# Kernel optimization log

Measured on AMD Instinct MI355X. Metric: run time of the kernel, lower is better.

Reference implementation:

```python
import math
import jax, jax.numpy as jnp
import numpy as np

B, C, H, W = 8, 512, 32, 32
NUM_HEADS = 8
HEAD_DIM = C // NUM_HEADS


def setup_inputs() -> dict:
    key = jax.random.key(0)
    ks = jax.random.split(key, 5)
    scale = 1.0 / math.sqrt(C)
    return {
        "x": jax.random.normal(ks[0], (B, C, H, W), dtype=jnp.float32),
        "Wq": jax.random.normal(ks[1], (C, C), dtype=jnp.float32) * scale,
        "bq": jnp.zeros((C,), dtype=jnp.float32),
        "Wk": jax.random.normal(ks[2], (C, C), dtype=jnp.float32) * scale,
        "bk": jnp.zeros((C,), dtype=jnp.float32),
        "Wv": jax.random.normal(ks[3], (C, C), dtype=jnp.float32) * scale,
        "bv": jnp.zeros((C,), dtype=jnp.float32),
        "Wo": jax.random.normal(ks[4], (C, C), dtype=jnp.float32) * scale,
        "bo": jnp.zeros((C,), dtype=jnp.float32),
    }


def reference(x, Wq, bq, Wk, bk, Wv, bv, Wo, bo):
    b, c, h, w = x.shape
    t = h * w
    # (B,C,H,W) -> (B,T,C) token sequence
    xt = x.reshape(b, c, t).transpose(0, 2, 1)
    Q = xt @ Wq + bq
    K = xt @ Wk + bk
    V = xt @ Wv + bv
    # (B,T,C) -> (B,nh,T,hd)
    def split_heads(z):
        return z.reshape(b, t, NUM_HEADS, HEAD_DIM).transpose(0, 2, 1, 3)
    Qh, Kh, Vh = split_heads(Q), split_heads(K), split_heads(V)
    S = jnp.einsum("bhqd,bhkd->bhqk", Qh, Kh) / math.sqrt(HEAD_DIM)
    A = jax.nn.softmax(S, axis=-1)  # dropout p=0.0 -> identity
    Y = jnp.einsum("bhqk,bhkd->bhqd", A, Vh)
    Y = Y.transpose(0, 2, 1, 3).reshape(b, t, c)
    O = Y @ Wo + bo
    out = xt + O
    return out.transpose(0, 2, 1).reshape(b, c, h, w)
```

## Files before the change

### kernel.cpp

```cpp
#include <hip/hip_runtime.h>
#include <hip/hip_bf16.h>

#define B_  8
#define C_  512
#define T_  1024
#define NH_ 8
#define HD_ 64

#define QSCALE 0.1803368801111243f

using short8 = __attribute__((ext_vector_type(8))) short;
using f32x4  = __attribute__((ext_vector_type(4))) float;
using f32x16 = __attribute__((ext_vector_type(16))) float;
using us4    = __attribute__((ext_vector_type(4))) unsigned short;

__device__ __forceinline__ unsigned short f2bf(float f) {
    unsigned u = __builtin_bit_cast(unsigned, f);
    u += 0x7fff + ((u >> 16) & 1);
    return (unsigned short)(u >> 16);
}
__device__ __forceinline__ unsigned pack2bf(float lo, float hi) {
    __hip_bfloat162 h = __float22bfloat162_rn(float2{lo, hi});
    unsigned u;
    __builtin_memcpy(&u, &h, 4);
    return u;
}

__device__ __forceinline__ void gload_lds16(const ushort* g, ushort* l) {
    __builtin_amdgcn_global_load_lds(
        (const __attribute__((address_space(1))) void*)g,
        (__attribute__((address_space(3))) void*)l, 16, 0, 0);
}

template <int N>
__device__ __forceinline__ void wait_vmcnt() {
    asm volatile("s_waitcnt vmcnt(%0)" ::"n"(N) : "memory");
    __builtin_amdgcn_sched_barrier(0);
}
__device__ __forceinline__ void barrier_raw() {
    __builtin_amdgcn_sched_barrier(0);
    __builtin_amdgcn_s_barrier();
}

__global__ __launch_bounds__(256) void k_prep(const float* __restrict__ x,
                                              const float* __restrict__ Wq,
                                              const float* __restrict__ Wk,
                                              const float* __restrict__ Wv,
                                              const float* __restrict__ Wo,
                                              ushort* __restrict__ xt,
                                              ushort* __restrict__ Wqkvt,
                                              ushort* __restrict__ Wot) {
    __shared__ float tile[32][33];
    int L = blockIdx.x;
    int tx = threadIdx.x & 31, ty = threadIdx.x >> 5;
    if (L < 4096) {
        int b = L >> 9, rem = L & 511;
        int t0 = (rem & 31) * 32, c0 = (rem >> 5) * 32;
#pragma unroll
        for (int i = 0; i < 4; i++)
            tile[ty + i * 8][tx] = x[((size_t)b * C_ + c0 + ty + i * 8) * T_ + t0 + tx];
        __syncthreads();
#pragma unroll
        for (int i = 0; i < 4; i++)
            xt[((size_t)b * T_ + t0 + ty + i * 8) * C_ + c0 + tx] = f2bf(tile[tx][ty + i * 8]);
    } else {
        int LL = L - 4096;
        int m = LL >> 8, rem = LL & 255;
        int k0 = (rem & 15) * 32, n0 = (rem >> 4) * 32;
        const float* W = (m == 0) ? Wq : (m == 1) ? Wk : (m == 2) ? Wv : Wo;
        ushort* dst = (m < 3) ? (Wqkvt + (size_t)m * C_ * C_) : Wot;
        float scale = (m == 0) ? QSCALE : 1.0f;
#pragma unroll
        for (int i = 0; i < 4; i++)
            tile[ty + i * 8][tx] = W[(size_t)(k0 + ty + i * 8) * C_ + n0 + tx];
        __syncthreads();
#pragma unroll
        for (int i = 0; i < 4; i++)
            dst[(size_t)(n0 + ty + i * 8) * C_ + k0 + tx] = f2bf(tile[tx][ty + i * 8] * scale);
    }
}

__device__ __forceinline__ void gemm_core(const ushort* __restrict__ A,
                                          const ushort* __restrict__ Bt,
                                          int row0, int col0, int tid,
                                          ushort (*As)[8192], ushort (*Bs)[8192],
                                          f32x4 acc[4][4]) {
    f32x4 zero = {0.f, 0.f, 0.f, 0.f};
#pragma unroll
    for (int i = 0; i < 4; i++)
#pragma unroll
        for (int j = 0; j < 4; j++) acc[i][j] = zero;
    int lane = tid & 63, w = tid >> 6;
    int ql = lane & 15, g = lane >> 4;
    int wm = (w >> 1) * 64, wn = (w & 1) * 64;
    int srow = lane >> 3;
    int scol8 = (lane & 7) ^ (srow & 7);

#pragma unroll
    for (int i = 0; i < 4; i++) {
        int c = w * 4 + i;
        int r = c * 8 + srow;
        gload_lds16(A + (size_t)(row0 + r) * C_ + scol8 * 8, As[0] + c * 512);
        gload_lds16(Bt + (size_t)(col0 + r) * C_ + scol8 * 8, Bs[0] + c * 512);
    }

#pragma unroll
    for (int kt = 0; kt < 8; kt++) {
        int cur = kt & 1;
        if (kt < 7) {
            int k0 = (kt + 1) * 64;
#pragma unroll
            for (int i = 0; i < 4; i++) {
                int c = w * 4 + i;
                int r = c * 8 + srow;
                gload_lds16(A + (size_t)(row0 + r) * C_ + k0 + scol8 * 8, As[cur ^ 1] + c * 512);
                gload_lds16(Bt + (size_t)(col0 + r) * C_ + k0 + scol8 * 8, Bs[cur ^ 1] + c * 512);
            }
            wait_vmcnt<8>();
        } else {
            wait_vmcnt<0>();
        }
        barrier_raw();
        const ushort* Ac = As[cur];
        const ushort* Bc = Bs[cur];
        __builtin_amdgcn_s_setprio(1);
#pragma unroll
        for (int s = 0; s < 2; s++) {
            short8 a[4], b[4];
            int cs = ((4 * s + g) ^ (ql & 7)) * 8;
#pragma unroll
            for (int mt = 0; mt < 4; mt++)
                a[mt] = *(const short8*)(Ac + (wm + mt * 16 + ql) * 64 + cs);
#pragma unroll
            for (int nt = 0; nt < 4; nt++)
                b[nt] = *(const short8*)(Bc + (wn + nt * 16 + ql) * 64 + cs);
#pragma unroll
            for (int mt = 0; mt < 4; mt++)
#pragma unroll
                for (int nt = 0; nt < 4; nt++)
                    acc[mt][nt] = __builtin_amdgcn_mfma_f32_16x16x32_bf16(
                        a[mt], b[nt], acc[mt][nt], 0, 0, 0);
        }
        __builtin_amdgcn_s_setprio(0);
        barrier_raw();
    }
}

__global__ __launch_bounds__(256) void k_qkv(const ushort* __restrict__ xt,
                                             const ushort* __restrict__ Wqkvt,
                                             const float* __restrict__ bq,
                                             const float* __restrict__ bk,
                                             const float* __restrict__ bv,
                                             ushort* __restrict__ Qh,
                                             ushort* __restrict__ Kh,
                                             ushort* __restrict__ Vt) {
    __shared__ __align__(16) ushort As[2][8192];
    __shared__ __align__(16) ushort Bs[2][8192];
    f32x4 acc[4][4];
    int tid = threadIdx.x;
    int L = blockIdx.x;
    int n = L >> 3, xcd = L & 7;
    int row0 = (xcd * 8 + (n & 7)) * 128;
    int col0 = (n >> 3) * 128;
    gemm_core(xt, Wqkvt, row0, col0, tid, As, Bs, acc);
    int lane = tid & 63, w = tid >> 6;
    int ql = lane & 15, g = lane >> 4;
    int wm = (w >> 1) * 64, wn = (w & 1) * 64;
    int which = col0 >> 9;
    const float* bias = (which == 0) ? bq : (which == 1) ? bk : bv;
    float bscale = (which == 0) ? QSCALE : 1.0f;
    ushort* Lt = &As[0][0];

    if (which < 3 && which != 2) {
        ushort* dst = (which == 0) ? Qh : Kh;
#pragma unroll
        for (int mt = 0; mt < 4; mt++)
#pragma unroll
            for (int nt = 0; nt < 4; nt++) {
                int col = wn + nt * 16 + ql;
                float bsv = bias[(col0 + col) & 511] * bscale;
#pragma unroll
                for (int r = 0; r < 4; r++) {
                    int row = wm + mt * 16 + 4 * g + r;
                    int sw = col ^ ((row & 7) << 3);
                    Lt[row * 128 + sw] = f2bf(acc[mt][nt][r] + bsv);
                }
            }
        __syncthreads();
#pragma unroll
        for (int i = 0; i < 8; i++) {
            int task = w * 512 + i * 64 + lane;
            int row = task >> 4, gran = task & 15;
            int sg = gran ^ (row & 7);
            short8 vle = *(const short8*)(Lt + row * 128 + sg * 8);
            int gcol = col0 + gran * 8;
            int hc = gcol & 511, h = hc >> 6, d = hc & 63;
            int grow = row0 + row, b = grow >> 10, t = grow & 1023;
            *(short8*)(dst + ((size_t)(b * NH_ + h) * T_ + t) * HD_ + d) = vle;
        }
    } else {
#pragma unroll
        for (int mt = 0; mt < 4; mt++)
#pragma unroll
            for (int nt = 0; nt < 4; nt++) {
                int col = wn + nt * 16 + ql;
                float bsv = bias[(col0 + col) & 511] * bscale;
                int rowb = wm + mt * 16 + 4 * g;
                int swz = (rowb >> 2) ^ (col & 31);
                us4 pk;
#pragma unroll
                for (int r = 0; r < 4; r++) pk[r] = f2bf(acc[mt][nt][r] + bsv);
                *(us4*)(Lt + col * 128 + swz * 4) = pk;
            }
        __syncthreads();
#pragma unroll
        for (int i = 0; i < 8; i++) {
            int task = w * 512 + i * 64 + lane;
            int colr = task >> 4, gran = task & 15;
            int g4a = (2 * gran) ^ (colr & 31);
            int g4b = (2 * gran + 1) ^ (colr & 31);
            us4 lo = *(const us4*)(Lt + colr * 128 + g4a * 4);
            us4 hi4 = *(const us4*)(Lt + colr * 128 + g4b * 4);
            us4 arr[2] = {lo, hi4};
            short8 vle;
            __builtin_memcpy(&vle, arr, 16);
            int gcol = col0 + colr;
            int hc = gcol & 511, h = hc >> 6, d = hc & 63;
            int grow = row0 + gran * 8, b = grow >> 10, t = grow & 1023;
            *(short8*)(Vt + ((size_t)(b * NH_ + h) * HD_ + d) * T_ + t) = vle;
        }
    }
}

__global__ __launch_bounds__(256) void k_attn(const ushort* __restrict__ Qh,
                                              const ushort* __restrict__ Kh,
                                              const ushort* __restrict__ Vt,
                                              ushort* __restrict__ Y) {
    __shared__ __align__(16) ushort KV[4][4096];
    int tid = threadIdx.x, lane = tid & 63, w = tid >> 6;
    int hi = lane >> 5, l31 = lane & 31, l7 = lane & 7;
    int bh = blockIdx.x & 63, q0 = (blockIdx.x >> 6) * 128;
    int b = bh >> 3, h = bh & 7;
    int srow = lane >> 3;
    int scol8 = l7 ^ (srow & 7);
    const ushort* Kbase = Kh + (size_t)bh * T_ * HD_;
    const ushort* Vbase = Vt + (size_t)bh * HD_ * T_;
    const ushort* kv = &KV[0][0];

    short8 qa[4];
#pragma unroll
    for (int s = 0; s < 4; s++)
        qa[s] = *(const short8*)(Qh + ((size_t)bh * T_ + q0 + w * 32 + l31) * HD_ +
                                 s * 16 + hi * 8);

    int fofs[4];
#pragma unroll
    for (int s = 0; s < 4; s++) fofs[s] = ((2 * s + hi) ^ l7) * 8;
    int rowlo = l31 * 64;

    short8 ones;
    {
        short ov = (l31 == 0) ? (short)0x3F80 : (short)0;
#pragma unroll
        for (int j = 0; j < 8; j++) ones[j] = ov;
    }

    f32x16 o0, o1, o5, z16;
#pragma unroll
    for (int i = 0; i < 16; i++) { o0[i] = 0.f; o1[i] = 0.f; o5[i] = 0.f; z16[i] = 0.f; }

#pragma unroll
    for (int i = 0; i < 2; i++) {
        int c = w * 2 + i;
        int r = c * 8 + srow;
        gload_lds16(Kbase + (size_t)r * HD_ + scol8 * 8, &KV[0][0] + c * 512);
        gload_lds16(Vbase + (size_t)r * T_ + scol8 * 8, &KV[2][0] + c * 512);
    }

#pragma unroll
    for (int t = 0; t < 16; t++) {
        const int cur = t & 1;
        if (t < 15) {
            int kv0 = (t + 1) * 64;
#pragma unroll
            for (int i = 0; i < 2; i++) {
                int c = w * 2 + i;
                int r = c * 8 + srow;
                gload_lds16(Kbase + (size_t)(kv0 + r) * HD_ + scol8 * 8,
                            &KV[cur ^ 1][0] + c * 512);
                gload_lds16(Vbase + (size_t)r * T_ + kv0 + scol8 * 8,
                            &KV[2 + (cur ^ 1)][0] + c * 512);
            }
            wait_vmcnt<4>();
        } else {
            wait_vmcnt<0>();
        }
        barrier_raw();

        f32x16 sT0, sT1;
        __builtin_amdgcn_s_setprio(1);
        {
            short8 ka0 = *(const short8*)(kv + cur * 4096 + rowlo + fofs[0]);
            short8 ka1 = *(const short8*)(kv + cur * 4096 + 2048 + rowlo + fofs[0]);
            sT0 = __builtin_amdgcn_mfma_f32_32x32x16_bf16(ka0, qa[0], z16, 0, 0, 0);
            sT1 = __builtin_amdgcn_mfma_f32_32x32x16_bf16(ka1, qa[0], z16, 0, 0, 0);
        }
#pragma unroll
        for (int s = 1; s < 4; s++) {
            short8 ka0 = *(const short8*)(kv + cur * 4096 + rowlo + fofs[s]);
            short8 ka1 = *(const short8*)(kv + cur * 4096 + 2048 + rowlo + fofs[s]);
            sT0 = __builtin_amdgcn_mfma_f32_32x32x16_bf16(ka0, qa[s], sT0, 0, 0, 0);
            sT1 = __builtin_amdgcn_mfma_f32_32x32x16_bf16(ka1, qa[s], sT1, 0, 0, 0);
        }
        __builtin_amdgcn_s_setprio(0);

        unsigned pkv0[8], pkv1[8];
#pragma unroll
        for (int i = 0; i < 8; i++) {
            pkv0[i] = pack2bf(__builtin_amdgcn_exp2f(sT0[2 * i]),
                              __builtin_amdgcn_exp2f(sT0[2 * i + 1]));
            pkv1[i] = pack2bf(__builtin_amdgcn_exp2f(sT1[2 * i]),
                              __builtin_amdgcn_exp2f(sT1[2 * i + 1]));
        }

        __builtin_amdgcn_s_setprio(1);
#pragma unroll
        for (int t4 = 0; t4 < 4; t4++) {
            const int h2 = t4 & 1;
            unsigned c0, c1, c2v, c3v;
            if (t4 < 2) {
                c0 = pkv0[4 * h2 + 0]; c2v = pkv0[4 * h2 + 2];
                c1 = pkv0[4 * h2 + 1]; c3v = pkv0[4 * h2 + 3];
            } else {
                c0 = pkv1[4 * h2 + 0]; c2v = pkv1[4 * h2 + 2];
                c1 = pkv1[4 * h2 + 1]; c3v = pkv1[4 * h2 + 3];
            }
            asm("v_permlane32_swap_b32 %0, %1" : "+v"(c0), "+v"(c2v));
            asm("v_permlane32_swap_b32 %0, %1" : "+v"(c1), "+v"(c3v));
            unsigned au[4] = {c0, c1, c2v, c3v};
            short8 pa;
            __builtin_memcpy(&pa, au, 16);
            short8 vb0 = *(const short8*)(kv + (2 + cur) * 4096 + rowlo + fofs[t4]);
            short8 vb1 = *(const short8*)(kv + (2 + cur) * 4096 + 2048 + rowlo + fofs[t4]);
            o0 = __builtin_amdgcn_mfma_f32_32x32x16_bf16(pa, vb0, o0, 0, 0, 0);
            o1 = __builtin_amdgcn_mfma_f32_32x32x16_bf16(pa, vb1, o1, 0, 0, 0);
            o5 = __builtin_amdgcn_mfma_f32_32x32x16_bf16(pa, ones, o5, 0, 0, 0);
        }
        __builtin_amdgcn_s_setprio(0);
        barrier_raw();
    }

#pragma unroll
    for (int r = 0; r < 16; r++) {
        float li = 1.0f / __shfl(o5[r], hi * 32);
        int qr = (r & 3) + 8 * (r >> 2) + 4 * hi;
        int trow = q0 + w * 32 + qr;
        size_t base = ((size_t)b * T_ + trow) * C_ + h * HD_;
        Y[base + l31] = f2bf(o0[r] * li);
        Y[base + 32 + l31] = f2bf(o1[r] * li);
    }
}

__global__ __launch_bounds__(256) void k_oproj(const ushort* __restrict__ Y,
                                               const ushort* __restrict__ Wot,
                                               const float* __restrict__ bo,
                                               const float* __restrict__ x,
                                               float* __restrict__ out) {
    __shared__ __align__(16) ushort As[2][8192];
    __shared__ __align__(16) ushort Bs[2][8192];
    f32x4 acc[4][4];
    int tid = threadIdx.x;
    int L = blockIdx.x;
    int n = L >> 3, xcd = L & 7;
    int row0 = (xcd * 8 + (n & 7)) * 128;
    int col0 = (n >> 3) * 128;
    gemm_core(Y, Wot, row0, col0, tid, As, Bs, acc);
    int lane = tid & 63, w = tid >> 6;
    int wm = (w >> 1) * 64, wn = (w & 1) * 64;
#pragma unroll
    for (int mt = 0; mt < 4; mt++) {
        int grow0 = row0 + wm + mt * 16 + ((lane >> 4) << 2);
        int b = grow0 >> 10, t = grow0 & 1023;
#pragma unroll
        for (int nt = 0; nt < 4; nt++) {
            int c = col0 + wn + nt * 16 + (lane & 15);
            float bsv = bo[c];
            size_t off = ((size_t)b * C_ + c) * T_ + t;
            float4 xv = *(const float4*)(x + off);
            float4 ov;
            ov.x = acc[mt][nt][0] + xv.x + bsv;
            ov.y = acc[mt][nt][1] + xv.y + bsv;
            ov.z = acc[mt][nt][2] + xv.z + bsv;
            ov.w = acc[mt][nt][3] + xv.w + bsv;
            *(float4*)(out + off) = ov;
        }
    }
}

extern "C" void kernel_launch(void* const* d_in, const int* in_sizes, int n_in,
                              void* d_out, int out_size, void* d_ws, size_t ws_size,
                              hipStream_t stream) {
    const float* x  = (const float*)d_in[0];
    const float* Wq = (const float*)d_in[1];
    const float* bq = (const float*)d_in[2];
    const float* Wk = (const float*)d_in[3];
    const float* bk = (const float*)d_in[4];
    const float* Wv = (const float*)d_in[5];
    const float* bv = (const float*)d_in[6];
    const float* Wo = (const float*)d_in[7];
    const float* bo = (const float*)d_in[8];
    float* out = (float*)d_out;

    char* ws = (char*)d_ws;
    ushort* xt    = (ushort*)(ws + 0);
    ushort* Wqkvt = (ushort*)(ws + 8388608);
    ushort* Wot   = (ushort*)(ws + 9961472);
    ushort* Qh    = (ushort*)(ws + 10485760);
    ushort* Kh    = (ushort*)(ws + 18874368);
    ushort* Vt    = (ushort*)(ws + 27262976);
    ushort* Yw    = xt;

    k_prep<<<dim3(5120), 256, 0, stream>>>(x, Wq, Wk, Wv, Wo, xt, Wqkvt, Wot);
    k_qkv<<<dim3(768), 256, 0, stream>>>(xt, Wqkvt, bq, bk, bv, Qh, Kh, Vt);
    k_attn<<<dim3(512), 256, 0, stream>>>(Qh, Kh, Vt, Yw);
    k_oproj<<<dim3(256), 256, 0, stream>>>(Yw, Wot, bo, x, out);
}
```

Before: 73.09 us.

## Deepen attention K/V prefetch to four LDS stages and drop trailing barrier

The attention kernel's K/V shared-memory ring grows from two stages to four, and loads are issued two tiles ahead instead of one, with vmcnt waits adjusted to match. With four slots and a two-tile lookahead, the second barrier at the end of each iteration is removed, since the slot being overwritten is no longer read by lagging waves. This aims to hide global load latency better and cut one barrier per tile, at the cost of doubling LDS use (64 KB per block), which may reduce how many blocks fit on a CU. A trivial simplification of a branch condition in the QKV projection is also included.

```diff
diff --git a/kernel.cpp b/kernel.cpp
--- a/kernel.cpp
+++ b/kernel.cpp
@@ -171,7 +171,7 @@
     float bscale = (which == 0) ? QSCALE : 1.0f;
     ushort* Lt = &As[0][0];
 
-    if (which < 3 && which != 2) {
+    if (which != 2) {
         ushort* dst = (which == 0) ? Qh : Kh;
 #pragma unroll
         for (int mt = 0; mt < 4; mt++)
@@ -236,7 +236,7 @@
                                               const ushort* __restrict__ Kh,
                                               const ushort* __restrict__ Vt,
                                               ushort* __restrict__ Y) {
-    __shared__ __align__(16) ushort KV[4][4096];
+    __shared__ __align__(16) ushort KV[8][4096];
     int tid = threadIdx.x, lane = tid & 63, w = tid >> 6;
     int hi = lane >> 5, l31 = lane & 31, l7 = lane & 7;
     int bh = blockIdx.x & 63, q0 = (blockIdx.x >> 6) * 128;
@@ -270,27 +270,35 @@
     for (int i = 0; i < 16; i++) { o0[i] = 0.f; o1[i] = 0.f; o5[i] = 0.f; z16[i] = 0.f; }
 
 #pragma unroll
-    for (int i = 0; i < 2; i++) {
-        int c = w * 2 + i;
-        int r = c * 8 + srow;
-        gload_lds16(Kbase + (size_t)r * HD_ + scol8 * 8, &KV[0][0] + c * 512);
-        gload_lds16(Vbase + (size_t)r * T_ + scol8 * 8, &KV[2][0] + c * 512);
+    for (int tt = 0; tt < 2; tt++) {
+#pragma unroll
+        for (int i = 0; i < 2; i++) {
+            int c = w * 2 + i;
+            int r = c * 8 + srow;
+            gload_lds16(Kbase + (size_t)(tt * 64 + r) * HD_ + scol8 * 8,
+                        &KV[tt][0] + c * 512);
+            gload_lds16(Vbase + (size_t)r * T_ + tt * 64 + scol8 * 8,
+                        &KV[4 + tt][0] + c * 512);
+        }
     }
 
 #pragma unroll
     for (int t = 0; t < 16; t++) {
-        const int cur = t & 1;
-        if (t < 15) {
-            int kv0 = (t + 1) * 64;
+        const int sl = t & 3;
+        if (t < 14) {
+            const int ds = (t + 2) & 3;
+            int kv0 = (t + 2) * 64;
 #pragma unroll
             for (int i = 0; i < 2; i++) {
                 int c = w * 2 + i;
                 int r = c * 8 + srow;
                 gload_lds16(Kbase + (size_t)(kv0 + r) * HD_ + scol8 * 8,
-                            &KV[cur ^ 1][0] + c * 512);
+                            &KV[ds][0] + c * 512);
                 gload_lds16(Vbase + (size_t)r * T_ + kv0 + scol8 * 8,
-                            &KV[2 + (cur ^ 1)][0] + c * 512);
+                            &KV[4 + ds][0] + c * 512);
             }
+            wait_vmcnt<8>();
+        } else if (t == 14) {
             wait_vmcnt<4>();
         } else {
             wait_vmcnt<0>();
@@ -300,15 +308,15 @@
         f32x16 sT0, sT1;
         __builtin_amdgcn_s_setprio(1);
         {
-            short8 ka0 = *(const short8*)(kv + cur * 4096 + rowlo + fofs[0]);
-            short8 ka1 = *(const short8*)(kv + cur * 4096 + 2048 + rowlo + fofs[0]);
+            short8 ka0 = *(const short8*)(kv + sl * 4096 + rowlo + fofs[0]);
+            short8 ka1 = *(const short8*)(kv + sl * 4096 + 2048 + rowlo + fofs[0]);
             sT0 = __builtin_amdgcn_mfma_f32_32x32x16_bf16(ka0, qa[0], z16, 0, 0, 0);
             sT1 = __builtin_amdgcn_mfma_f32_32x32x16_bf16(ka1, qa[0], z16, 0, 0, 0);
         }
 #pragma unroll
         for (int s = 1; s < 4; s++) {
-            short8 ka0 = *(const short8*)(kv + cur * 4096 + rowlo + fofs[s]);
-            short8 ka1 = *(const short8*)(kv + cur * 4096 + 2048 + rowlo + fofs[s]);
+            short8 ka0 = *(const short8*)(kv + sl * 4096 + rowlo + fofs[s]);
+            short8 ka1 = *(const short8*)(kv + sl * 4096 + 2048 + rowlo + fofs[s]);
             sT0 = __builtin_amdgcn_mfma_f32_32x32x16_bf16(ka0, qa[s], sT0, 0, 0, 0);
             sT1 = __builtin_amdgcn_mfma_f32_32x32x16_bf16(ka1, qa[s], sT1, 0, 0, 0);
         }
@@ -340,14 +348,13 @@
             unsigned au[4] = {c0, c1, c2v, c3v};
             short8 pa;
             __builtin_memcpy(&pa, au, 16);
-            short8 vb0 = *(const short8*)(kv + (2 + cur) * 4096 + rowlo + fofs[t4]);
-            short8 vb1 = *(const short8*)(kv + (2 + cur) * 4096 + 2048 + rowlo + fofs[t4]);
+            short8 vb0 = *(const short8*)(kv + (4 + sl) * 4096 + rowlo + fofs[t4]);
+            short8 vb1 = *(const short8*)(kv + (4 + sl) * 4096 + 2048 + rowlo + fofs[t4]);
             o0 = __builtin_amdgcn_mfma_f32_32x32x16_bf16(pa, vb0, o0, 0, 0, 0);
             o1 = __builtin_amdgcn_mfma_f32_32x32x16_bf16(pa, vb1, o1, 0, 0, 0);
             o5 = __builtin_amdgcn_mfma_f32_32x32x16_bf16(pa, ones, o5, 0, 0, 0);
         }
         __builtin_amdgcn_s_setprio(0);
-        barrier_raw();
     }
 
 #pragma unroll
```

After: 73.26 us. About the same (+0.2%).
